# Kernel tuning notes

Hardware: AMD Instinct MI355X
Metric: run time of the kernel (lower is better)

The kernel has to match this reference:

```python
import jax, jax.numpy as jnp
import numpy as np

NEG_INF = -1e10


def setup_inputs() -> dict:
    key = jax.random.key(0)
    ks = jax.random.split(key, 9)
    B, S, H, E = 64, 4096, 512, 512
    hidden = jax.random.normal(ks[0], (B, H), dtype=jnp.float32)
    encoder_outputs = jax.random.normal(ks[1], (B, S, E), dtype=jnp.float32)
    mask = jax.random.randint(ks[2], (B, S), 0, 2, dtype=jnp.int32)
    s = 1.0 / np.sqrt(H)
    Wq = jax.random.uniform(ks[3], (H, H), jnp.float32, -s, s)
    bq = jax.random.uniform(ks[4], (H,), jnp.float32, -s, s)
    se = 1.0 / np.sqrt(E)
    Wk = jax.random.uniform(ks[5], (E, H), jnp.float32, -se, se)
    bk = jax.random.uniform(ks[6], (H,), jnp.float32, -se, se)
    Wv = jax.random.uniform(ks[7], (H, 1), jnp.float32, -s, s)
    bv = jax.random.uniform(ks[8], (1,), jnp.float32, -s, s)
    return {"hidden": hidden, "encoder_outputs": encoder_outputs, "mask": mask,
            "Wq": Wq, "bq": bq, "Wk": Wk, "bk": bk, "Wv": Wv, "bv": bv}


def reference(hidden, encoder_outputs, mask, Wq, bq, Wk, bk, Wv, bv):
    # query projection: (B, H) -> broadcast over src_len
    q = hidden @ Wq + bq                       # (B, H)
    k = jnp.einsum('bse,eh->bsh', encoder_outputs, Wk) + bk  # (B, S, H)
    energy = jnp.tanh(q[:, None, :] + k)       # (B, S, H)
    scores = jnp.einsum('bsh,h->bs', energy, Wv[:, 0]) + bv[0]  # (B, S)
    scores = jnp.where(mask == 0, NEG_INF, scores)
    attn = jax.nn.softmax(scores, axis=1)      # (B, S)
    context = jnp.einsum('bs,bse->be', attn, encoder_outputs)   # (B, E)
    return context, attn
```

## Files before the change

kernel.cpp:

```cpp
#include <hip/hip_runtime.h>
#include <hip/hip_bf16.h>

#define B_ 64
#define S_ 4096
#define H_ 512
#define E_ 512
#define NEG_INF_ -1e10f

typedef __attribute__((ext_vector_type(8))) short short8;
typedef __attribute__((ext_vector_type(16))) float f32x16;

static __device__ __forceinline__ unsigned short f2bf(float f) {
    union { float f; unsigned u; } v; v.f = f;
    unsigned x = v.u;
    x += 0x7FFFu + ((x >> 16) & 1u);
    return (unsigned short)(x >> 16);
}

static __device__ __forceinline__ unsigned pk2(float lo, float hi) {
    float2 f; f.x = lo; f.y = hi;
    union { __hip_bfloat162 h; unsigned u; } c;
    c.h = __float22bfloat162_rn(f);
    return c.u;
}

static __device__ __forceinline__ void gload_lds16(const void* g, void* l) {
    __builtin_amdgcn_global_load_lds(
        (const __attribute__((address_space(1))) void*)g,
        (__attribute__((address_space(3))) void*)l, 16, 0, 0);
}

#define VMCNT6 do { asm volatile("s_waitcnt vmcnt(6)" ::: "memory"); __builtin_amdgcn_sched_barrier(0); } while (0)
#define VMCNT0 do { asm volatile("s_waitcnt vmcnt(0)" ::: "memory"); __builtin_amdgcn_sched_barrier(0); } while (0)
#define LGKM0  do { asm volatile("s_waitcnt lgkmcnt(0)" ::: "memory"); __builtin_amdgcn_sched_barrier(0); } while (0)

__global__ void prep_wkt(const float* __restrict__ wk, unsigned short* __restrict__ wkt) {
    int idx = blockIdx.x * 256 + threadIdx.x;
    int h = idx >> 9, e = idx & 511;
    wkt[idx] = f2bf(wk[e * H_ + h]);
}

__global__ void prep_qb(const float* __restrict__ hidden, const float* __restrict__ wq,
                        const float* __restrict__ bq, const float* __restrict__ bk,
                        float* __restrict__ qb) {
    __shared__ float hid[H_];
    int b = blockIdx.x, t = threadIdx.x;
    hid[t]       = hidden[b * H_ + t];
    hid[t + 256] = hidden[b * H_ + t + 256];
    __syncthreads();
    for (int hh = t; hh < H_; hh += 256) {
        float s = 0.f;
        for (int e = 0; e < H_; ++e) s += hid[e] * wq[e * H_ + hh];
        qb[b * H_ + hh] = s + bq[hh] + bk[hh];
    }
}

__global__ __launch_bounds__(256, 3) void scores_kernel(
    const float* __restrict__ enc, const unsigned short* __restrict__ wkt,
    const float* __restrict__ qb, const float* __restrict__ wv,
    float* __restrict__ part)
{
    __shared__ char lds[40960];

    int id = blockIdx.x;
    int xcd = id & 7, qq = id >> 3;
    int logical = xcd * 1024 + qq;
    int b  = logical >> 7;
    int r  = logical & 127;
    int st = r >> 2, nt = r & 3;
    int s0 = st * 128;

    const int tid  = threadIdx.x;
    const int lane = tid & 63;
    const int wave = tid >> 6;
    const int wr   = wave >> 1;
    const int wc   = wave & 1;
    const int l31  = lane & 31;
    const int g    = lane >> 5;

    const float* encb = enc + ((size_t)b * S_ + s0) * E_;

    auto loadA = [&](int kc, float4 (&rg)[4]) {
#pragma unroll
        for (int j = 0; j < 2; ++j) {
            int sid = tid * 2 + j;
            int row = sid >> 2, ksl = sid & 3;
            const float* p = encb + (size_t)row * 512 + kc * 32 + ksl * 8;
            rg[j * 2 + 0] = *(const float4*)p;
            rg[j * 2 + 1] = *(const float4*)(p + 4);
        }
    };
    auto writeA = [&](char* buf, const float4 (&rg)[4]) {
#pragma unroll
        for (int j = 0; j < 2; ++j) {
            int sid = tid * 2 + j;
            int row = sid >> 2, ksl = sid & 3;
            int srow = row & 31;
            int sst  = ((row >> 5) * 4 + ksl) ^ (srow & 15);
            union { short8 s; unsigned u[4]; } u;
            u.u[0] = pk2(rg[j * 2].x, rg[j * 2].y);
            u.u[1] = pk2(rg[j * 2].z, rg[j * 2].w);
            u.u[2] = pk2(rg[j * 2 + 1].x, rg[j * 2 + 1].y);
            u.u[3] = pk2(rg[j * 2 + 1].z, rg[j * 2 + 1].w);
            *(short8*)(buf + srow * 256 + sst * 16) = u.s;
        }
    };
    auto stageB = [&](int kc, char* buf) {
#pragma unroll
        for (int p = 0; p < 2; ++p) {
            int gi0 = p * 256 + wave * 64;
            char* db = buf + gi0 * 16;
            int gi = gi0 + lane;
            int sn = gi >> 4, ss = gi & 15;
            int sl = ss ^ (sn & 15);
            int n  = (sl >> 2) * 32 + sn;
            const unsigned short* gp = wkt + (size_t)(nt * 128 + n) * 512 + kc * 32 + (sl & 3) * 8;
            gload_lds16(gp, db);
        }
    };

    f32x16 acc[2][2];
#pragma unroll
    for (int mr = 0; mr < 2; ++mr)
#pragma unroll
        for (int nf = 0; nf < 2; ++nf)
#pragma unroll
            for (int e = 0; e < 16; ++e) acc[mr][nf][e] = 0.f;

    float4 ra[4], rb[4];

    loadA(0, ra); stageB(0, lds + 16384);
    loadA(1, rb); stageB(1, lds + 16384 + 8192);

    auto iter = [&](int kc, float4 (&rg)[4]) {
        if (kc < 15) { VMCNT6; } else { VMCNT0; }
        char* Ab = lds + (kc & 1) * 8192;
        writeA(Ab, rg);
        LGKM0;
        __builtin_amdgcn_s_barrier();
        __builtin_amdgcn_sched_barrier(0);
        if (kc < 14) {
            loadA(kc + 2, rg);
            stageB(kc + 2, lds + 16384 + ((kc + 2) % 3) * 8192);
        }
        const char* Bb = lds + 16384 + (kc % 3) * 8192;
#pragma unroll
        for (int ks = 0; ks < 2; ++ks) {
            short8 af[2], bf[2];
#pragma unroll
            for (int mr = 0; mr < 2; ++mr) {
                int slog = (wr * 2 + mr) * 4 + ks * 2 + g;
                af[mr] = *(const short8*)(Ab + l31 * 256 + ((slog ^ (l31 & 15)) << 4));
            }
#pragma unroll
            for (int nf = 0; nf < 2; ++nf) {
                int sl = (wc * 2 + nf) * 4 + ks * 2 + g;
                bf[nf] = *(const short8*)(Bb + l31 * 256 + ((sl ^ (l31 & 15)) << 4));
            }
            acc[0][0] = __builtin_amdgcn_mfma_f32_32x32x16_bf16(af[0], bf[0], acc[0][0], 0, 0, 0);
            acc[0][1] = __builtin_amdgcn_mfma_f32_32x32x16_bf16(af[0], bf[1], acc[0][1], 0, 0, 0);
            acc[1][0] = __builtin_amdgcn_mfma_f32_32x32x16_bf16(af[1], bf[0], acc[1][0], 0, 0, 0);
            acc[1][1] = __builtin_amdgcn_mfma_f32_32x32x16_bf16(af[1], bf[1], acc[1][1], 0, 0, 0);
        }
    };

    for (int t2 = 0; t2 < 8; ++t2) {
        iter(t2 * 2,     ra);
        iter(t2 * 2 + 1, rb);
    }

    float p[2][16];
#pragma unroll
    for (int nf = 0; nf < 2; ++nf) {
        int col = nt * 128 + wc * 64 + nf * 32 + l31;
        float qv  = qb[b * H_ + col];
        float wvv = wv[col];
#pragma unroll
        for (int mr = 0; mr < 2; ++mr)
#pragma unroll
            for (int e = 0; e < 16; ++e) {
                float x  = qv + acc[mr][nf][e];
                float ex = __expf(2.f * x);
                float th = 1.f - 2.f / (ex + 1.f);
                float v  = wvv * th;
                p[mr][e] = nf ? (p[mr][e] + v) : v;
            }
    }

    __syncthreads();
    float* ps = (float*)lds;
#pragma unroll
    for (int mr = 0; mr < 2; ++mr)
#pragma unroll
        for (int e = 0; e < 16; ++e) {
            int row = mr * 32 + (e & 3) + 8 * (e >> 2) + 4 * g;
            ps[(wave * 64 + row) * 36 + l31] = p[mr][e];
        }
    __syncthreads();
    float rsum = 0.f;
    {
        const float* myrow = ps + (size_t)(wave * 64 + lane) * 36;
#pragma unroll
        for (int j = 0; j < 8; ++j) {
            float4 v = *(const float4*)(myrow + j * 4);
            rsum += (v.x + v.y) + (v.z + v.w);
        }
    }
    float* pf = (float*)(lds + 36864);
    pf[wave * 64 + lane] = rsum;
    __syncthreads();
    if (tid < 128) {
        int wr2 = tid >> 6, rr = tid & 63;
        float v = pf[(wr2 * 2 + 0) * 64 + rr] + pf[(wr2 * 2 + 1) * 64 + rr];
        int s = s0 + wr2 * 64 + rr;
        part[((size_t)b * S_ + s) * 4 + nt] = v;
    }
}

__global__ void softmax_kernel(const float* __restrict__ part, const int* __restrict__ mask,
                               const float* __restrict__ bvp, float* __restrict__ attn) {
    __shared__ float red[8];
    int b = blockIdx.x, tid = threadIdx.x;
    int wid = tid >> 6, lane = tid & 63;
    float bv0 = bvp[0];
    float vals[8];
    float mx = -3.4e38f;
#pragma unroll
    for (int i = 0; i < 8; ++i) {
        int s = i * 512 + tid;
        float4 v = *(const float4*)(part + ((size_t)b * S_ + s) * 4);
        float sc = (v.x + v.y) + (v.z + v.w) + bv0;
        sc = mask[(size_t)b * S_ + s] ? sc : NEG_INF_;
        vals[i] = sc;
        mx = fmaxf(mx, sc);
    }
#pragma unroll
    for (int off = 1; off < 64; off <<= 1) mx = fmaxf(mx, __shfl_xor(mx, off));
    if (lane == 0) red[wid] = mx;
    __syncthreads();
    mx = red[0];
#pragma unroll
    for (int w = 1; w < 8; ++w) mx = fmaxf(mx, red[w]);
    __syncthreads();
    float sum = 0.f;
#pragma unroll
    for (int i = 0; i < 8; ++i) { vals[i] = __expf(vals[i] - mx); sum += vals[i]; }
#pragma unroll
    for (int off = 1; off < 64; off <<= 1) sum += __shfl_xor(sum, off);
    if (lane == 0) red[wid] = sum;
    __syncthreads();
    sum = red[0] + red[1] + red[2] + red[3] + red[4] + red[5] + red[6] + red[7];
    float inv = 1.f / sum;
#pragma unroll
    for (int i = 0; i < 8; ++i) attn[(size_t)b * S_ + i * 512 + tid] = vals[i] * inv;
}

__global__ void ctx_partial(const float* __restrict__ attn, const float* __restrict__ enc,
                            float* __restrict__ part) {
    __shared__ float a[256];
    int c = blockIdx.x, b = blockIdx.y, t = threadIdx.x;
    a[t] = attn[(size_t)b * S_ + c * 256 + t];
    __syncthreads();
    const float* ep = enc + (size_t)b * S_ * E_ + (size_t)c * 256 * E_ + t * 2;
    float x = 0.f, y = 0.f;
#pragma unroll 4
    for (int s = 0; s < 256; ++s) {
        float2 v = *(const float2*)(ep + (size_t)s * E_);
        x += a[s] * v.x;
        y += a[s] * v.y;
    }
    float* o = part + ((size_t)c * B_ + b) * E_ + t * 2;
    o[0] = x; o[1] = y;
}

__global__ void ctx_reduce(const float* __restrict__ part, float* __restrict__ ctx) {
    int idx = blockIdx.x * 256 + threadIdx.x;
    float s = 0.f;
#pragma unroll
    for (int c = 0; c < 16; ++c) s += part[(size_t)c * (B_ * E_) + idx];
    ctx[idx] = s;
}

extern "C" void kernel_launch(void* const* d_in, const int* in_sizes, int n_in,
                              void* d_out, int out_size, void* d_ws, size_t ws_size,
                              hipStream_t stream) {
    const float* hidden = (const float*)d_in[0];
    const float* enc    = (const float*)d_in[1];
    const int*   mask   = (const int*)d_in[2];
    const float* Wq     = (const float*)d_in[3];
    const float* bq     = (const float*)d_in[4];
    const float* Wk     = (const float*)d_in[5];
    const float* bk     = (const float*)d_in[6];
    const float* Wv     = (const float*)d_in[7];
    const float* bv     = (const float*)d_in[8];

    float* out  = (float*)d_out;
    char*  ws   = (char*)d_ws;
    float*          qbuf   = (float*)ws;
    unsigned short* wkt    = (unsigned short*)(ws + 131072);
    float*          pscore = (float*)(ws + 655360);
    float*          cpart  = (float*)(ws + 655360);

    float* ctx  = out;
    float* attn = out + B_ * E_;

    prep_wkt<<<1024, 256, 0, stream>>>(Wk, wkt);
    prep_qb<<<64, 256, 0, stream>>>(hidden, Wq, bq, bk, qbuf);
    scores_kernel<<<8192, 256, 0, stream>>>(enc, wkt, qbuf, Wv, pscore);
    softmax_kernel<<<64, 512, 0, stream>>>(pscore, mask, bv, attn);
    ctx_partial<<<dim3(16, 64), 256, 0, stream>>>(attn, enc, cpart);
    ctx_reduce<<<128, 256, 0, stream>>>(cpart, ctx);
}
```

Measured before the change: 441.9 us.

## Remap A-tile loads to per-row contiguous chunks and raise occupancy

Each thread now loads 16 contiguous floats of one encoder row (row = tid&127) instead of two 8-float slices, with precomputed LDS write addresses and a rotation-based swizzle replacing the XOR swizzle for A. The K loop is fully unrolled, B staging is issued before A loads, MFMA sections run at raised wave priority via s_setprio, and launch bounds go from 3 to 4 blocks per CU. The aim is fewer address computations, better global load coalescing per thread and more latency hiding through occupancy. The tighter register budget and full unroll risk spills or changed LDS bank conflict behaviour.

```diff
diff --git a/kernel.cpp b/kernel.cpp
--- a/kernel.cpp
+++ b/kernel.cpp
@@ -55,7 +55,7 @@
     }
 }
 
-__global__ __launch_bounds__(256, 3) void scores_kernel(
+__global__ __launch_bounds__(256, 4) void scores_kernel(
     const float* __restrict__ enc, const unsigned short* __restrict__ wkt,
     const float* __restrict__ qb, const float* __restrict__ wv,
     float* __restrict__ part)
@@ -80,30 +80,29 @@
 
     const float* encb = enc + ((size_t)b * S_ + s0) * E_;
 
-    auto loadA = [&](int kc, float4 (&rg)[4]) {
-#pragma unroll
-        for (int j = 0; j < 2; ++j) {
-            int sid = tid * 2 + j;
-            int row = sid >> 2, ksl = sid & 3;
-            const float* p = encb + (size_t)row * 512 + kc * 32 + ksl * 8;
-            rg[j * 2 + 0] = *(const float4*)p;
-            rg[j * 2 + 1] = *(const float4*)(p + 4);
-        }
+    const int arow   = tid & 127;
+    const int aksl0  = (tid >> 7) * 2;
+    const float* aptr = encb + (size_t)arow * 512 + aksl0 * 8;
+    const int asrow  = arow & 31;
+    const int aslb   = (arow >> 5) * 4 + aksl0;
+    char* const awb0 = (char*)0 + asrow * 256 + (((aslb + 0 + asrow) & 15) << 4);
+    char* const awb1 = (char*)0 + asrow * 256 + (((aslb + 1 + asrow) & 15) << 4);
+
+    auto loadA = [&](int kc, float4 (&st_)[4]) {
+        const float* p = aptr + kc * 32;
+        st_[0] = *(const float4*)(p);
+        st_[1] = *(const float4*)(p + 4);
+        st_[2] = *(const float4*)(p + 8);
+        st_[3] = *(const float4*)(p + 12);
     };
-    auto writeA = [&](char* buf, const float4 (&rg)[4]) {
-#pragma unroll
-        for (int j = 0; j < 2; ++j) {
-            int sid = tid * 2 + j;
-            int row = sid >> 2, ksl = sid & 3;
-            int srow = row & 31;
-            int sst  = ((row >> 5) * 4 + ksl) ^ (srow & 15);
-            union { short8 s; unsigned u[4]; } u;
-            u.u[0] = pk2(rg[j * 2].x, rg[j * 2].y);
-            u.u[1] = pk2(rg[j * 2].z, rg[j * 2].w);
-            u.u[2] = pk2(rg[j * 2 + 1].x, rg[j * 2 + 1].y);
-            u.u[3] = pk2(rg[j * 2 + 1].z, rg[j * 2 + 1].w);
-            *(short8*)(buf + srow * 256 + sst * 16) = u.s;
-        }
+    auto writeA = [&](char* buf, const float4 (&st_)[4]) {
+        union { short8 s; unsigned u[4]; } u0, u1;
+        u0.u[0] = pk2(st_[0].x, st_[0].y); u0.u[1] = pk2(st_[0].z, st_[0].w);
+        u0.u[2] = pk2(st_[1].x, st_[1].y); u0.u[3] = pk2(st_[1].z, st_[1].w);
+        u1.u[0] = pk2(st_[2].x, st_[2].y); u1.u[1] = pk2(st_[2].z, st_[2].w);
+        u1.u[2] = pk2(st_[3].x, st_[3].y); u1.u[3] = pk2(st_[3].z, st_[3].w);
+        *(short8*)(buf + (size_t)awb0) = u0.s;
+        *(short8*)(buf + (size_t)awb1) = u1.s;
     };
     auto stageB = [&](int kc, char* buf) {
 #pragma unroll
@@ -129,28 +128,30 @@
 
     float4 ra[4], rb[4];
 
-    loadA(0, ra); stageB(0, lds + 16384);
-    loadA(1, rb); stageB(1, lds + 16384 + 8192);
-
-    auto iter = [&](int kc, float4 (&rg)[4]) {
+    stageB(0, lds + 16384);          loadA(0, ra);
+    stageB(1, lds + 16384 + 8192);   loadA(1, rb);
+
+#pragma unroll
+    for (int kc = 0; kc < 16; ++kc) {
         if (kc < 15) { VMCNT6; } else { VMCNT0; }
         char* Ab = lds + (kc & 1) * 8192;
-        writeA(Ab, rg);
+        if (kc & 1) writeA(Ab, rb); else writeA(Ab, ra);
         LGKM0;
         __builtin_amdgcn_s_barrier();
         __builtin_amdgcn_sched_barrier(0);
         if (kc < 14) {
-            loadA(kc + 2, rg);
             stageB(kc + 2, lds + 16384 + ((kc + 2) % 3) * 8192);
+            if (kc & 1) loadA(kc + 2, rb); else loadA(kc + 2, ra);
         }
         const char* Bb = lds + 16384 + (kc % 3) * 8192;
+        __builtin_amdgcn_s_setprio(1);
 #pragma unroll
         for (int ks = 0; ks < 2; ++ks) {
             short8 af[2], bf[2];
 #pragma unroll
             for (int mr = 0; mr < 2; ++mr) {
-                int slog = (wr * 2 + mr) * 4 + ks * 2 + g;
-                af[mr] = *(const short8*)(Ab + l31 * 256 + ((slog ^ (l31 & 15)) << 4));
+                int sl = (wr * 2 + mr) * 4 + ks * 2 + g;
+                af[mr] = *(const short8*)(Ab + l31 * 256 + (((sl + l31) & 15) << 4));
             }
 #pragma unroll
             for (int nf = 0; nf < 2; ++nf) {
@@ -162,11 +163,7 @@
             acc[1][0] = __builtin_amdgcn_mfma_f32_32x32x16_bf16(af[1], bf[0], acc[1][0], 0, 0, 0);
             acc[1][1] = __builtin_amdgcn_mfma_f32_32x32x16_bf16(af[1], bf[1], acc[1][1], 0, 0, 0);
         }
-    };
-
-    for (int t2 = 0; t2 < 8; ++t2) {
-        iter(t2 * 2,     ra);
-        iter(t2 * 2 + 1, rb);
+        __builtin_amdgcn_s_setprio(0);
     }
 
     float p[2][16];
```

Measured after the change: 506.5 us. 14.6% more time.

## Replace triple-buffered async K-loop with single-buffer 64-wide K steps

Applied to the files above, without the earlier changes.

Rewrites the scores GEMM main loop. Each step now covers 64 of K instead of 32, runs 8 iterations instead of 16, and uses single LDS buffers for A and B guarded by two __syncthreads. The hand-placed vmcnt/lgkmcnt waits and the three-slot B ring are removed, and LDS shrinks slightly. This halves barrier count and simplifies scheduling, but B is now loaded via global_load_lds right before the barrier with no prefetch, so its latency is exposed each iteration, and the A register prefetch doubles in size.

```diff
diff --git a/kernel.cpp b/kernel.cpp
--- a/kernel.cpp
+++ b/kernel.cpp
@@ -29,10 +29,6 @@
         (const __attribute__((address_space(1))) void*)g,
         (__attribute__((address_space(3))) void*)l, 16, 0, 0);
 }
-
-#define VMCNT6 do { asm volatile("s_waitcnt vmcnt(6)" ::: "memory"); __builtin_amdgcn_sched_barrier(0); } while (0)
-#define VMCNT0 do { asm volatile("s_waitcnt vmcnt(0)" ::: "memory"); __builtin_amdgcn_sched_barrier(0); } while (0)
-#define LGKM0  do { asm volatile("s_waitcnt lgkmcnt(0)" ::: "memory"); __builtin_amdgcn_sched_barrier(0); } while (0)
 
 __global__ void prep_wkt(const float* __restrict__ wk, unsigned short* __restrict__ wkt) {
     int idx = blockIdx.x * 256 + threadIdx.x;
@@ -60,7 +56,7 @@
     const float* __restrict__ qb, const float* __restrict__ wv,
     float* __restrict__ part)
 {
-    __shared__ char lds[40960];
+    __shared__ char lds[38912];
 
     int id = blockIdx.x;
     int xcd = id & 7, qq = id >> 3;
@@ -80,42 +76,53 @@
 
     const float* encb = enc + ((size_t)b * S_ + s0) * E_;
 
-    auto loadA = [&](int kc, float4 (&rg)[4]) {
+    auto loadA = [&](int kc, float4 (&rg)[8]) {
 #pragma unroll
         for (int j = 0; j < 2; ++j) {
             int sid = tid * 2 + j;
             int row = sid >> 2, ksl = sid & 3;
-            const float* p = encb + (size_t)row * 512 + kc * 32 + ksl * 8;
-            rg[j * 2 + 0] = *(const float4*)p;
-            rg[j * 2 + 1] = *(const float4*)(p + 4);
+            const float* pr = encb + (size_t)row * 512 + kc * 64 + ksl * 8;
+#pragma unroll
+            for (int kk = 0; kk < 2; ++kk) {
+                rg[j * 4 + kk * 2 + 0] = *(const float4*)(pr + kk * 32);
+                rg[j * 4 + kk * 2 + 1] = *(const float4*)(pr + kk * 32 + 4);
+            }
         }
     };
-    auto writeA = [&](char* buf, const float4 (&rg)[4]) {
+    auto writeA = [&](const float4 (&rg)[8]) {
 #pragma unroll
         for (int j = 0; j < 2; ++j) {
             int sid = tid * 2 + j;
             int row = sid >> 2, ksl = sid & 3;
             int srow = row & 31;
             int sst  = ((row >> 5) * 4 + ksl) ^ (srow & 15);
-            union { short8 s; unsigned u[4]; } u;
-            u.u[0] = pk2(rg[j * 2].x, rg[j * 2].y);
-            u.u[1] = pk2(rg[j * 2].z, rg[j * 2].w);
-            u.u[2] = pk2(rg[j * 2 + 1].x, rg[j * 2 + 1].y);
-            u.u[3] = pk2(rg[j * 2 + 1].z, rg[j * 2 + 1].w);
-            *(short8*)(buf + srow * 256 + sst * 16) = u.s;
+#pragma unroll
+            for (int kk = 0; kk < 2; ++kk) {
+                const float4& a = rg[j * 4 + kk * 2 + 0];
+                const float4& c = rg[j * 4 + kk * 2 + 1];
+                union { short8 s; unsigned u[4]; } u;
+                u.u[0] = pk2(a.x, a.y); u.u[1] = pk2(a.z, a.w);
+                u.u[2] = pk2(c.x, c.y); u.u[3] = pk2(c.z, c.w);
+                *(short8*)(lds + kk * 8192 + srow * 256 + sst * 16) = u.s;
+            }
         }
     };
-    auto stageB = [&](int kc, char* buf) {
-#pragma unroll
-        for (int p = 0; p < 2; ++p) {
-            int gi0 = p * 256 + wave * 64;
-            char* db = buf + gi0 * 16;
-            int gi = gi0 + lane;
-            int sn = gi >> 4, ss = gi & 15;
-            int sl = ss ^ (sn & 15);
-            int n  = (sl >> 2) * 32 + sn;
-            const unsigned short* gp = wkt + (size_t)(nt * 128 + n) * 512 + kc * 32 + (sl & 3) * 8;
-            gload_lds16(gp, db);
+    auto stageB = [&](int kc) {
+#pragma unroll
+        for (int kk = 0; kk < 2; ++kk) {
+            char* buf = lds + 16384 + kk * 8192;
+#pragma unroll
+            for (int p = 0; p < 2; ++p) {
+                int gi0 = p * 256 + wave * 64;
+                char* db = buf + gi0 * 16;
+                int gi = gi0 + lane;
+                int sn = gi >> 4, ss = gi & 15;
+                int sl = ss ^ (sn & 15);
+                int n  = (sl >> 2) * 32 + sn;
+                const unsigned short* gp =
+                    wkt + (size_t)(nt * 128 + n) * 512 + kc * 64 + kk * 32 + (sl & 3) * 8;
+                gload_lds16(gp, db);
+            }
         }
     };
 
@@ -127,46 +134,36 @@
 #pragma unroll
             for (int e = 0; e < 16; ++e) acc[mr][nf][e] = 0.f;
 
-    float4 ra[4], rb[4];
-
-    loadA(0, ra); stageB(0, lds + 16384);
-    loadA(1, rb); stageB(1, lds + 16384 + 8192);
-
-    auto iter = [&](int kc, float4 (&rg)[4]) {
-        if (kc < 15) { VMCNT6; } else { VMCNT0; }
-        char* Ab = lds + (kc & 1) * 8192;
-        writeA(Ab, rg);
-        LGKM0;
-        __builtin_amdgcn_s_barrier();
-        __builtin_amdgcn_sched_barrier(0);
-        if (kc < 14) {
-            loadA(kc + 2, rg);
-            stageB(kc + 2, lds + 16384 + ((kc + 2) % 3) * 8192);
-        }
-        const char* Bb = lds + 16384 + (kc % 3) * 8192;
-#pragma unroll
-        for (int ks = 0; ks < 2; ++ks) {
+    float4 ar[8];
+    loadA(0, ar);
+
+    for (int kc = 0; kc < 8; ++kc) {
+        __syncthreads();
+        writeA(ar);
+        stageB(kc);
+        __syncthreads();
+        if (kc < 7) loadA(kc + 1, ar);
+        const char* Ap = lds;
+        const char* Bp = lds + 16384;
+#pragma unroll
+        for (int kst = 0; kst < 4; ++kst) {
+            const int kk = kst >> 1, ks = kst & 1;
             short8 af[2], bf[2];
 #pragma unroll
             for (int mr = 0; mr < 2; ++mr) {
-                int slog = (wr * 2 + mr) * 4 + ks * 2 + g;
-                af[mr] = *(const short8*)(Ab + l31 * 256 + ((slog ^ (l31 & 15)) << 4));
+                int sl = (wr * 2 + mr) * 4 + ks * 2 + g;
+                af[mr] = *(const short8*)(Ap + kk * 8192 + l31 * 256 + ((sl ^ (l31 & 15)) << 4));
             }
 #pragma unroll
             for (int nf = 0; nf < 2; ++nf) {
                 int sl = (wc * 2 + nf) * 4 + ks * 2 + g;
-                bf[nf] = *(const short8*)(Bb + l31 * 256 + ((sl ^ (l31 & 15)) << 4));
+                bf[nf] = *(const short8*)(Bp + kk * 8192 + l31 * 256 + ((sl ^ (l31 & 15)) << 4));
             }
             acc[0][0] = __builtin_amdgcn_mfma_f32_32x32x16_bf16(af[0], bf[0], acc[0][0], 0, 0, 0);
             acc[0][1] = __builtin_amdgcn_mfma_f32_32x32x16_bf16(af[0], bf[1], acc[0][1], 0, 0, 0);
             acc[1][0] = __builtin_amdgcn_mfma_f32_32x32x16_bf16(af[1], bf[0], acc[1][0], 0, 0, 0);
             acc[1][1] = __builtin_amdgcn_mfma_f32_32x32x16_bf16(af[1], bf[1], acc[1][1], 0, 0, 0);
         }
-    };
-
-    for (int t2 = 0; t2 < 8; ++t2) {
-        iter(t2 * 2,     ra);
-        iter(t2 * 2 + 1, rb);
     }
 
     float p[2][16];
```

Result: faster. 421.7 us (median of 2 runs) (-4.6%).

## Replace deep register/LDS prefetch pipeline with simple double-buffered loop

Applied to the files above, without the earlier changes.

Replaces the two-register-set A prefetch and triple-buffered B staging, which used hand-placed vmcnt/lgkmcnt waits, with a plain double-buffered loop that has one __syncthreads per K chunk. The next A chunk is loaded, converted to bf16 and written to LDS right after the MFMAs instead of two iterations ahead. The A LDS swizzle changes from XOR to an additive rotation, and the LDS allocation shrinks. This simplifies synchronisation, but global load latency for A is now less hidden because each load is consumed in the same iteration.

```diff
diff --git a/kernel.cpp b/kernel.cpp
--- a/kernel.cpp
+++ b/kernel.cpp
@@ -29,10 +29,6 @@
         (const __attribute__((address_space(1))) void*)g,
         (__attribute__((address_space(3))) void*)l, 16, 0, 0);
 }
-
-#define VMCNT6 do { asm volatile("s_waitcnt vmcnt(6)" ::: "memory"); __builtin_amdgcn_sched_barrier(0); } while (0)
-#define VMCNT0 do { asm volatile("s_waitcnt vmcnt(0)" ::: "memory"); __builtin_amdgcn_sched_barrier(0); } while (0)
-#define LGKM0  do { asm volatile("s_waitcnt lgkmcnt(0)" ::: "memory"); __builtin_amdgcn_sched_barrier(0); } while (0)
 
 __global__ void prep_wkt(const float* __restrict__ wk, unsigned short* __restrict__ wkt) {
     int idx = blockIdx.x * 256 + threadIdx.x;
@@ -60,7 +56,7 @@
     const float* __restrict__ qb, const float* __restrict__ wv,
     float* __restrict__ part)
 {
-    __shared__ char lds[40960];
+    __shared__ char lds[38912];
 
     int id = blockIdx.x;
     int xcd = id & 7, qq = id >> 3;
@@ -80,29 +76,37 @@
 
     const float* encb = enc + ((size_t)b * S_ + s0) * E_;
 
+    const int sid0  = tid * 2;
+    const int arow0 = sid0 >> 2;
     auto loadA = [&](int kc, float4 (&rg)[4]) {
 #pragma unroll
         for (int j = 0; j < 2; ++j) {
-            int sid = tid * 2 + j;
+            int sid = sid0 + j;
             int row = sid >> 2, ksl = sid & 3;
             const float* p = encb + (size_t)row * 512 + kc * 32 + ksl * 8;
             rg[j * 2 + 0] = *(const float4*)p;
             rg[j * 2 + 1] = *(const float4*)(p + 4);
         }
     };
-    auto writeA = [&](char* buf, const float4 (&rg)[4]) {
+    auto cvtA = [&](const float4 (&rg)[4], short8 (&ab)[2]) {
 #pragma unroll
         for (int j = 0; j < 2; ++j) {
-            int sid = tid * 2 + j;
-            int row = sid >> 2, ksl = sid & 3;
-            int srow = row & 31;
-            int sst  = ((row >> 5) * 4 + ksl) ^ (srow & 15);
             union { short8 s; unsigned u[4]; } u;
             u.u[0] = pk2(rg[j * 2].x, rg[j * 2].y);
             u.u[1] = pk2(rg[j * 2].z, rg[j * 2].w);
             u.u[2] = pk2(rg[j * 2 + 1].x, rg[j * 2 + 1].y);
             u.u[3] = pk2(rg[j * 2 + 1].z, rg[j * 2 + 1].w);
-            *(short8*)(buf + srow * 256 + sst * 16) = u.s;
+            ab[j] = u.s;
+        }
+    };
+    auto writeA = [&](char* buf, const short8 (&ab)[2]) {
+#pragma unroll
+        for (int j = 0; j < 2; ++j) {
+            int sid = sid0 + j;
+            int row = sid >> 2, ksl = sid & 3;
+            int srow = row & 31;
+            int sst  = (((row >> 5) * 4 + ksl) + srow) & 15;
+            *(short8*)(buf + srow * 256 + sst * 16) = ab[j];
         }
     };
     auto stageB = [&](int kc, char* buf) {
@@ -127,46 +131,42 @@
 #pragma unroll
             for (int e = 0; e < 16; ++e) acc[mr][nf][e] = 0.f;
 
-    float4 ra[4], rb[4];
-
-    loadA(0, ra); stageB(0, lds + 16384);
-    loadA(1, rb); stageB(1, lds + 16384 + 8192);
-
-    auto iter = [&](int kc, float4 (&rg)[4]) {
-        if (kc < 15) { VMCNT6; } else { VMCNT0; }
-        char* Ab = lds + (kc & 1) * 8192;
-        writeA(Ab, rg);
-        LGKM0;
-        __builtin_amdgcn_s_barrier();
-        __builtin_amdgcn_sched_barrier(0);
-        if (kc < 14) {
-            loadA(kc + 2, rg);
-            stageB(kc + 2, lds + 16384 + ((kc + 2) % 3) * 8192);
-        }
-        const char* Bb = lds + 16384 + (kc % 3) * 8192;
+    float4 arf[4];
+    short8 abf[2];
+
+    loadA(0, arf);
+    cvtA(arf, abf);
+    stageB(0, lds + 16384);
+    writeA(lds, abf);
+
+    for (int kc = 0; kc < 16; ++kc) {
+        __syncthreads();
+        if (kc < 15) stageB(kc + 1, lds + 16384 + ((kc + 1) & 1) * 8192);
+        const char* Ap = lds + (kc & 1) * 8192;
+        const char* Bp = lds + 16384 + (kc & 1) * 8192;
 #pragma unroll
         for (int ks = 0; ks < 2; ++ks) {
             short8 af[2], bf[2];
 #pragma unroll
             for (int mr = 0; mr < 2; ++mr) {
-                int slog = (wr * 2 + mr) * 4 + ks * 2 + g;
-                af[mr] = *(const short8*)(Ab + l31 * 256 + ((slog ^ (l31 & 15)) << 4));
+                int sl = (wr * 2 + mr) * 4 + ks * 2 + g;
+                af[mr] = *(const short8*)(Ap + l31 * 256 + (((sl + l31) & 15) << 4));
             }
 #pragma unroll
             for (int nf = 0; nf < 2; ++nf) {
                 int sl = (wc * 2 + nf) * 4 + ks * 2 + g;
-                bf[nf] = *(const short8*)(Bb + l31 * 256 + ((sl ^ (l31 & 15)) << 4));
+                bf[nf] = *(const short8*)(Bp + l31 * 256 + ((sl ^ (l31 & 15)) << 4));
             }
             acc[0][0] = __builtin_amdgcn_mfma_f32_32x32x16_bf16(af[0], bf[0], acc[0][0], 0, 0, 0);
             acc[0][1] = __builtin_amdgcn_mfma_f32_32x32x16_bf16(af[0], bf[1], acc[0][1], 0, 0, 0);
             acc[1][0] = __builtin_amdgcn_mfma_f32_32x32x16_bf16(af[1], bf[0], acc[1][0], 0, 0, 0);
             acc[1][1] = __builtin_amdgcn_mfma_f32_32x32x16_bf16(af[1], bf[1], acc[1][1], 0, 0, 0);
         }
-    };
-
-    for (int t2 = 0; t2 < 8; ++t2) {
-        iter(t2 * 2,     ra);
-        iter(t2 * 2 + 1, rb);
+        if (kc < 15) {
+            loadA(kc + 1, arf);
+            cvtA(arf, abf);
+            writeA(lds + ((kc + 1) & 1) * 8192, abf);
+        }
     }
 
     float p[2][16];
```

After: 425.9 us. 1.04x faster.
